# Kernel optimization log

Hardware: AMD Instinct MI355X
Metric: run time of the kernel (lower is better)

The kernel has to match this reference:

```python
import jax, jax.numpy as jnp
import numpy as np

B, N = 16, 8192

# batched gather: pts [N,C], ind [S,K] -> [S,K,C]
_bgather = jax.vmap(lambda pts, ind: pts[ind])


def _fps(xyz, npoint):
    """Farthest point sampling. xyz [B,N,3] -> idx [B,npoint] int32."""
    b, n, _ = xyz.shape
    def step(carry, _):
        mind, last = carry
        p = jax.vmap(lambda pts, i: pts[i])(xyz, last)  # [B,3]
        d = jnp.sum((xyz - p[:, None, :]) ** 2, axis=-1)  # [B,N]
        mind = jnp.minimum(mind, d)
        nxt = jnp.argmax(mind, axis=-1).astype(jnp.int32)
        return (mind, nxt), last
    init = (jnp.full((b, n), 1e10, xyz.dtype), jnp.zeros((b,), jnp.int32))
    _, idx = jax.lax.scan(step, init, None, length=npoint)
    return jnp.transpose(idx)  # [B,npoint]


def _ball_query(xyz, new_xyz, radius, nsample):
    """xyz [B,N,3], new_xyz [B,S,3] -> idx [B,S,nsample] int32.
    First nsample points within radius; slots past the count filled with first hit
    (matches pointnet2 CUDA ball_query semantics)."""
    n = xyz.shape[1]
    # squared distances without materializing [B,S,N,3]
    d2 = (jnp.sum(new_xyz ** 2, -1)[:, :, None]
          + jnp.sum(xyz ** 2, -1)[:, None, :]
          - 2.0 * jnp.einsum('bsc,bnc->bsn', new_xyz, xyz))  # [B,S,N]
    key = jnp.where(d2 < radius * radius, jnp.arange(n, dtype=jnp.int32), n)
    idx = jnp.sort(key, axis=-1)[..., :nsample]  # first in-radius indices
    first = idx[..., :1]
    idx = jnp.where(idx == n, first, idx)  # pad with first hit
    return jnp.clip(idx, 0, n - 1)


def _mlp(g, layers):
    # g [B,S,K,C]; shared 1x1-conv MLP with folded BN, ReLU
    for W, b in layers:
        g = jax.nn.relu(jnp.einsum('bskc,oc->bsko', g, W) + b)
    return g


def _sa(xyz, feat, npoint, radius, nsample, layers):
    fidx = _fps(xyz, npoint)
    new_xyz = _bgather(xyz, fidx)  # [B,S,3]
    idx = _ball_query(xyz, new_xyz, radius, nsample)  # [B,S,K]
    g = _bgather(xyz, idx) - new_xyz[:, :, None, :]  # centered grouped xyz
    if feat is not None:
        g = jnp.concatenate([g, _bgather(feat, idx)], axis=-1)
    g = _mlp(g, layers)
    return new_xyz, jnp.max(g, axis=2)  # [B,S,Cout]


def setup_inputs() -> dict:
    key = jax.random.key(0)
    ks = jax.random.split(key, 13)
    def w(k, o, i):
        return (jax.random.normal(k, (o, i), jnp.float32) * 0.1)
    inp = {
        'x': jax.random.uniform(ks[0], (B, N, 3), jnp.float32),
        'W1a': w(ks[1], 64, 3),    'b1a': jnp.zeros((64,), jnp.float32),
        'W1b': w(ks[2], 128, 64),  'b1b': jnp.zeros((128,), jnp.float32),
        'W2a': w(ks[3], 128, 131), 'b2a': jnp.zeros((128,), jnp.float32),
        'W2b': w(ks[4], 256, 128), 'b2b': jnp.zeros((256,), jnp.float32),
        'W3a': w(ks[5], 512, 259), 'b3a': jnp.zeros((512,), jnp.float32),
        'W3b': w(ks[6], 1024, 512),'b3b': jnp.zeros((1024,), jnp.float32),
    }
    return inp


def reference(x, W1a, b1a, W1b, b1b, W2a, b2a, W2b, b2b, W3a, b3a, W3b, b3b):
    xyz = x[..., 0:3]  # input_feat_dim=0 -> no extra features
    # sa1: npoint=512, r=0.2, k=64, mlp 3->64->128 (use_xyz)
    xyz1, feat1 = _sa(xyz, None, 512, 0.2, 64, [(W1a, b1a), (W1b, b1b)])
    # sa2: npoint=128, r=0.4, k=64, mlp 131->128->256
    xyz2, feat2 = _sa(xyz1, feat1, 128, 0.4, 64, [(W2a, b2a), (W2b, b2b)])
    # sa3: group-all, mlp 259->512->1024
    g = jnp.concatenate([xyz2, feat2], axis=-1)[:, None]  # [B,1,128,259]
    g = _mlp(g, [(W3a, b3a), (W3b, b3b)])
    return jnp.max(g, axis=2)[:, 0]  # [B,1024]
```

## Files before the change

kernel.cpp:

```cpp
#include <hip/hip_runtime.h>

#define B 16
#define N 8192
#define S1 512
#define S2 128
#define K 64

template<int CTRL>
__device__ __forceinline__ float dpp_max_f32(float v) {
  unsigned o = (unsigned)__builtin_amdgcn_update_dpp(
      (int)__float_as_uint(v), (int)__float_as_uint(v), CTRL, 0xF, 0xF, false);
  return fmaxf(v, __uint_as_float(o));
}

__device__ __forceinline__ float wave_max_bcast(float v) {
  v = dpp_max_f32<0x111>(v);
  v = dpp_max_f32<0x112>(v);
  v = dpp_max_f32<0x114>(v);
  v = dpp_max_f32<0x118>(v);
  v = dpp_max_f32<0x142>(v);
  v = dpp_max_f32<0x143>(v);
  return __uint_as_float((unsigned)__builtin_amdgcn_readlane(
      (int)__float_as_uint(v), 63));
}

template<int NT, int PT, int MAXP, int MAXN>
__device__ __forceinline__ void fps_body(
    const float* __restrict__ pts, float* __restrict__ out_xyz,
    float* __restrict__ out2, int out2_stride, int n, int npoint) {
  const int b = blockIdx.x;
  const int t = threadIdx.x;
  const int w = t >> 6;
  const float* base = pts + (size_t)b * n * 3;
  __shared__ unsigned long long cell[3][4];
  __shared__ float s_out[MAXP * 3];
  __shared__ float s_pts[MAXN * 3];
  if (t < 12) ((unsigned long long*)cell)[t] = 0ull;
  float px[PT], py[PT], pz[PT], mind[PT];
#pragma unroll
  for (int i = 0; i < PT; i++) {
    int p = t + i * NT;
    px[i] = base[p * 3 + 0];
    py[i] = base[p * 3 + 1];
    pz[i] = base[p * 3 + 2];
    mind[i] = 1e10f;
    s_pts[p * 3 + 0] = px[i];
    s_pts[p * 3 + 1] = py[i];
    s_pts[p * 3 + 2] = pz[i];
  }
  float cx = base[0], cy = base[1], cz = base[2];
  __syncthreads();
  for (int it = 0; it < npoint; it++) {
    if (t == 0) {
      s_out[it * 3 + 0] = cx; s_out[it * 3 + 1] = cy; s_out[it * 3 + 2] = cz;
    }
    float bv = -1.0f;
#pragma unroll
    for (int i = 0; i < PT; i++) {
      float dx = px[i] - cx, dy = py[i] - cy, dz = pz[i] - cz;
      float d = dx * dx;
      d = fmaf(dy, dy, d);
      d = fmaf(dz, dz, d);
      float md = fminf(mind[i], d);
      mind[i] = md;
      bv = fmaxf(bv, md);
    }
    float gm = wave_max_bcast(bv);
    if (bv == gm) {
      int bi = 0;
#pragma unroll
      for (int i = PT - 1; i >= 0; i--)
        if (mind[i] == bv) bi = i;
      unsigned long long kk = ((unsigned long long)__float_as_uint(bv) << 32) |
                              (~(unsigned)(t + bi * NT));
      atomicMax(&cell[it % 3][w & 3], kk);
    }
    if (t < 4) cell[(it + 1) % 3][t] = 0ull;
    __syncthreads();
    unsigned long long k0 = cell[it % 3][0];
    unsigned long long k1 = cell[it % 3][1];
    unsigned long long k2 = cell[it % 3][2];
    unsigned long long k3 = cell[it % 3][3];
    unsigned long long wk = k0 > k1 ? k0 : k1;
    unsigned long long wk2 = k2 > k3 ? k2 : k3;
    if (wk2 > wk) wk = wk2;
    int ui = __builtin_amdgcn_readfirstlane((int)(~(unsigned)wk));
    const float* q = s_pts + ui * 3;
    cx = q[0]; cy = q[1]; cz = q[2];
  }
  for (int e = t; e < npoint * 3; e += NT)
    out_xyz[(size_t)b * npoint * 3 + e] = s_out[e];
  if (out2) {
    for (int e = t; e < npoint; e += NT) {
      float* o2 = out2 + ((size_t)b * npoint + e) * out2_stride;
      o2[0] = s_out[e * 3 + 0];
      o2[1] = s_out[e * 3 + 1];
      o2[2] = s_out[e * 3 + 2];
    }
  }
}

__global__ __launch_bounds__(1024) __attribute__((amdgpu_waves_per_eu(4, 4)))
void fps1_kernel(const float* __restrict__ pts, float* __restrict__ out_xyz,
                 float* __restrict__ out2, int out2_stride, int n, int npoint) {
  fps_body<1024, 8, 512, 8192>(pts, out_xyz, out2, out2_stride, n, npoint);
}

template<int PT, int MAXP, int MAXN>
__global__ __launch_bounds__(64) __attribute__((amdgpu_waves_per_eu(1, 1)))
void fps_wave_kernel(const float* __restrict__ pts, float* __restrict__ out_xyz,
                     float* __restrict__ out2, int out2_stride, int n, int npoint) {
  const int b = blockIdx.x;
  const int t = threadIdx.x;
  const float* base = pts + (size_t)b * n * 3;
  __shared__ unsigned long long cell[2];
  __shared__ float s_out[MAXP * 3];
  __shared__ float s_pts[MAXN * 3];
  if (t < 2) cell[t] = 0ull;
  float px[PT], py[PT], pz[PT], mind[PT];
#pragma unroll
  for (int i = 0; i < PT; i++) {
    int p = t + i * 64;
    px[i] = base[p * 3 + 0];
    py[i] = base[p * 3 + 1];
    pz[i] = base[p * 3 + 2];
    mind[i] = 1e10f;
    s_pts[p * 3 + 0] = px[i];
    s_pts[p * 3 + 1] = py[i];
    s_pts[p * 3 + 2] = pz[i];
  }
  float cx = base[0], cy = base[1], cz = base[2];
  for (int it = 0; it < npoint; it++) {
    if (t == 0) {
      s_out[it * 3 + 0] = cx; s_out[it * 3 + 1] = cy; s_out[it * 3 + 2] = cz;
    }
    float bv = -1.0f;
#pragma unroll
    for (int i = 0; i < PT; i++) {
      float dx = px[i] - cx, dy = py[i] - cy, dz = pz[i] - cz;
      float d = dx * dx;
      d = fmaf(dy, dy, d);
      d = fmaf(dz, dz, d);
      float md = fminf(mind[i], d);
      mind[i] = md;
      bv = fmaxf(bv, md);
    }
    float gm = wave_max_bcast(bv);
    if (bv == gm) {
      int bi = 0;
#pragma unroll
      for (int i = PT - 1; i >= 0; i--)
        if (mind[i] == bv) bi = i;
      unsigned long long kk = ((unsigned long long)__float_as_uint(bv) << 32) |
                              (~(unsigned)(t + bi * 64));
      atomicMax(&cell[it & 1], kk);
    }
    __threadfence_block();
    unsigned long long wk = cell[it & 1];
    if (t == 0) cell[(it + 1) & 1] = 0ull;
    int ui = __builtin_amdgcn_readfirstlane((int)(~(unsigned)wk));
    const float* q = s_pts + ui * 3;
    cx = q[0]; cy = q[1]; cz = q[2];
  }
  for (int e = t; e < npoint * 3; e += 64)
    out_xyz[(size_t)b * npoint * 3 + e] = s_out[e];
  if (out2) {
    for (int e = t; e < npoint; e += 64) {
      float* o2 = out2 + ((size_t)b * npoint + e) * out2_stride;
      o2[0] = s_out[e * 3 + 0];
      o2[1] = s_out[e * 3 + 1];
      o2[2] = s_out[e * 3 + 2];
    }
  }
}

__global__ __launch_bounds__(256) void ballq_kernel(
    const float* __restrict__ pts, const float* __restrict__ ctr,
    int* __restrict__ idx, int n, int ns, int total, float r2) {
  int gid = blockIdx.x * blockDim.x + threadIdx.x;
  int wid = gid >> 6;
  int lane = threadIdx.x & 63;
  if (wid >= total) return;
  int b = wid / ns, s = wid - b * ns;
  const float* pb = pts + (size_t)b * n * 3;
  const float* c = ctr + ((size_t)b * ns + s) * 3;
  float cx = c[0], cy = c[1], cz = c[2];
  float sc = cx * cx + cy * cy + cz * cz;
  int* out = idx + ((size_t)b * ns + s) * K;
  int cnt = 0, first = n - 1;
  for (int base = 0; base < n && cnt < K; base += 64) {
    int p = base + lane;
    float x = pb[p * 3 + 0], y = pb[p * 3 + 1], z = pb[p * 3 + 2];
    float sp = x * x + y * y + z * z;
    float dot = cx * x + cy * y + cz * z;
    float d2 = sc + sp - 2.0f * dot;
    bool inr = d2 < r2;
    unsigned long long m = __ballot(inr);
    if (cnt == 0 && m != 0ull) first = base + __ffsll((long long)m) - 1;
    int pre = (int)__popcll(m & ((1ull << lane) - 1ull));
    if (inr && (cnt + pre) < K) out[cnt + pre] = p;
    cnt += (int)__popcll(m);
  }
  if (cnt > K) cnt = K;
  if (lane >= cnt) out[lane] = first;
}

__global__ __launch_bounds__(256) void sa1_kernel(
    const float* __restrict__ xyz, const int* __restrict__ idx,
    const float* __restrict__ ctr, const float* __restrict__ W1a,
    const float* __restrict__ b1a, const float* __restrict__ W1b,
    const float* __restrict__ b1b, float* __restrict__ feat) {
  __shared__ float s_l[K][3];
  __shared__ float s_h[K][64];
  __shared__ float s_red[128];
  int blk = blockIdx.x;
  int b = blk >> 9, s = blk & 511;
  int tid = threadIdx.x;
  const int* gi = idx + ((size_t)b * S1 + s) * K;
  const float* c = ctr + ((size_t)b * S1 + s) * 3;
  float cx = c[0], cy = c[1], cz = c[2];
  if (tid < K) {
    int p = gi[tid];
    const float* q = xyz + ((size_t)b * N + p) * 3;
    s_l[tid][0] = q[0] - cx;
    s_l[tid][1] = q[1] - cy;
    s_l[tid][2] = q[2] - cz;
  }
  __syncthreads();
  for (int e = tid; e < K * 64; e += 256) {
    int k = e >> 6, o = e & 63;
    float v = b1a[o] + W1a[o * 3 + 0] * s_l[k][0] + W1a[o * 3 + 1] * s_l[k][1] +
              W1a[o * 3 + 2] * s_l[k][2];
    s_h[k][o] = fmaxf(v, 0.f);
  }
  __syncthreads();
  int o = tid & 127, half = tid >> 7;
  float w[64];
  const float4* wp = (const float4*)(W1b + o * 64);
#pragma unroll
  for (int c4 = 0; c4 < 16; c4++) {
    float4 t4 = wp[c4];
    w[c4 * 4 + 0] = t4.x; w[c4 * 4 + 1] = t4.y;
    w[c4 * 4 + 2] = t4.z; w[c4 * 4 + 3] = t4.w;
  }
  float bias = b1b[o];
  float m = -1e30f;
  int k0 = half * 32;
  for (int k = k0; k < k0 + 32; k++) {
    float acc = bias;
    const float4* hp = (const float4*)(&s_h[k][0]);
#pragma unroll
    for (int c4 = 0; c4 < 16; c4++) {
      float4 h = hp[c4];
      acc = fmaf(h.x, w[c4 * 4 + 0], acc);
      acc = fmaf(h.y, w[c4 * 4 + 1], acc);
      acc = fmaf(h.z, w[c4 * 4 + 2], acc);
      acc = fmaf(h.w, w[c4 * 4 + 3], acc);
    }
    m = fmaxf(m, acc);
  }
  if (half == 1) s_red[o] = m;
  __syncthreads();
  if (half == 0) {
    m = fmaxf(m, s_red[o]);
    feat[((size_t)b * S1 + s) * 128 + o] = fmaxf(m, 0.f);
  }
}

__global__ __launch_bounds__(256) void sa2_kernel(
    const float* __restrict__ xyz1, const float* __restrict__ feat1,
    const int* __restrict__ idx, const float* __restrict__ ctr,
    const float* __restrict__ W2a, const float* __restrict__ b2a,
    const float* __restrict__ W2b, const float* __restrict__ b2b,
    float* __restrict__ in3) {
  __shared__ int s_pi[K];
  __shared__ float s_g[K][132];
  __shared__ float s_h[K][128];
  __shared__ float s_red[256];
  int blk = blockIdx.x;
  int b = blk >> 7, s = blk & 127;
  int tid = threadIdx.x;
  const int* gi = idx + ((size_t)b * S2 + s) * K;
  const float* c = ctr + ((size_t)b * S2 + s) * 3;
  float cx = c[0], cy = c[1], cz = c[2];
  if (tid < K) {
    int p = gi[tid];
    s_pi[tid] = p;
    const float* q = xyz1 + ((size_t)b * S1 + p) * 3;
    s_g[tid][0] = q[0] - cx;
    s_g[tid][1] = q[1] - cy;
    s_g[tid][2] = q[2] - cz;
  }
  __syncthreads();
  for (int e = tid; e < K * 128; e += 256) {
    int k = e >> 7, f = e & 127;
    s_g[k][3 + f] = feat1[((size_t)b * S1 + s_pi[k]) * 128 + f];
  }
  __syncthreads();
  {
    int o = tid & 127, half = tid >> 7, k0 = half * 32;
    const float* wr = W2a + o * 131;
    float acc[32];
    float bias = b2a[o];
#pragma unroll
    for (int j = 0; j < 32; j++) acc[j] = bias;
    for (int c4 = 0; c4 < 32; c4++) {
      float w0 = wr[c4 * 4 + 0], w1 = wr[c4 * 4 + 1];
      float w2 = wr[c4 * 4 + 2], w3 = wr[c4 * 4 + 3];
#pragma unroll
      for (int j = 0; j < 32; j++) {
        float4 g = *(const float4*)(&s_g[k0 + j][c4 * 4]);
        acc[j] = fmaf(g.x, w0, acc[j]);
        acc[j] = fmaf(g.y, w1, acc[j]);
        acc[j] = fmaf(g.z, w2, acc[j]);
        acc[j] = fmaf(g.w, w3, acc[j]);
      }
    }
    float w0 = wr[128], w1 = wr[129], w2 = wr[130];
#pragma unroll
    for (int j = 0; j < 32; j++) {
      acc[j] = fmaf(s_g[k0 + j][128], w0, acc[j]);
      acc[j] = fmaf(s_g[k0 + j][129], w1, acc[j]);
      acc[j] = fmaf(s_g[k0 + j][130], w2, acc[j]);
      s_h[k0 + j][o] = fmaxf(acc[j], 0.f);
    }
  }
  __syncthreads();
  {
    int oa = tid & 127, half = tid >> 7, k0 = half * 32;
    const float4* wpa = (const float4*)(W2b + oa * 128);
    const float4* wpb = (const float4*)(W2b + (oa + 128) * 128);
    float acca[32], accb[32];
    float ba = b2b[oa], bb = b2b[oa + 128];
#pragma unroll
    for (int j = 0; j < 32; j++) { acca[j] = ba; accb[j] = bb; }
    for (int c4 = 0; c4 < 32; c4++) {
      float4 wa = wpa[c4];
      float4 wb = wpb[c4];
#pragma unroll
      for (int j = 0; j < 32; j++) {
        float4 h = *(const float4*)(&s_h[k0 + j][c4 * 4]);
        acca[j] = fmaf(h.x, wa.x, acca[j]);
        acca[j] = fmaf(h.y, wa.y, acca[j]);
        acca[j] = fmaf(h.z, wa.z, acca[j]);
        acca[j] = fmaf(h.w, wa.w, acca[j]);
        accb[j] = fmaf(h.x, wb.x, accb[j]);
        accb[j] = fmaf(h.y, wb.y, accb[j]);
        accb[j] = fmaf(h.z, wb.z, accb[j]);
        accb[j] = fmaf(h.w, wb.w, accb[j]);
      }
    }
    float ma = -1e30f, mb = -1e30f;
#pragma unroll
    for (int j = 0; j < 32; j++) { ma = fmaxf(ma, acca[j]); mb = fmaxf(mb, accb[j]); }
    if (half == 1) { s_red[oa] = ma; s_red[oa + 128] = mb; }
    __syncthreads();
    if (half == 0) {
      ma = fmaxf(ma, s_red[oa]);
      mb = fmaxf(mb, s_red[oa + 128]);
      float* o3 = &in3[((size_t)b * S2 + s) * 259 + 3];
      o3[oa] = fmaxf(ma, 0.f);
      o3[oa + 128] = fmaxf(mb, 0.f);
    }
  }
}

__global__ __launch_bounds__(256) void mlp3a_kernel(
    const float* __restrict__ in3, const float* __restrict__ W3a,
    const float* __restrict__ b3a, float* __restrict__ h3) {
  __shared__ float s_wt[64][65];
  __shared__ float s_a[64][64];
  int blk = blockIdx.x;
  int b = blk >> 4, r = blk & 15;
  int ot = r >> 1, sh = r & 1;
  int tid = threadIdx.x;
  int o = tid & 63, sq = tid >> 6;
  float acc[16];
  float bias = b3a[ot * 64 + o];
#pragma unroll
  for (int j = 0; j < 16; j++) acc[j] = bias;
  for (int ch = 0; ch < 5; ch++) {
    int cb = ch * 64;
    int len = (ch == 4) ? 3 : 64;
    for (int e = tid; e < 4096; e += 256) {
      int oo = e >> 6, cc = e & 63;
      if (cc < len) s_wt[cc][oo] = W3a[(size_t)(ot * 64 + oo) * 259 + cb + cc];
    }
    for (int e = tid; e < 4096; e += 256) {
      int ss = e >> 6, cc = e & 63;
      if (cc < len) s_a[ss][cc] = in3[((size_t)b * S2 + sh * 64 + ss) * 259 + cb + cc];
    }
    __syncthreads();
    for (int cc = 0; cc < len; cc++) {
      float wv = s_wt[cc][o];
#pragma unroll
      for (int j = 0; j < 16; j++)
        acc[j] = fmaf(wv, s_a[sq * 16 + j][cc], acc[j]);
    }
    __syncthreads();
  }
#pragma unroll
  for (int j = 0; j < 16; j++) {
    int s = sh * 64 + sq * 16 + j;
    h3[((size_t)b * S2 + s) * 512 + ot * 64 + o] = fmaxf(acc[j], 0.f);
  }
}

__global__ __launch_bounds__(256) void mlp3b_kernel(
    const float* __restrict__ h3, const float* __restrict__ W3b,
    const float* __restrict__ b3b, float* __restrict__ out) {
  __shared__ float s_wt[64][65];
  __shared__ float s_h[128][64];
  __shared__ float s_red[4][64];
  int blk = blockIdx.x;
  int b = blk >> 4, ot = blk & 15;
  int tid = threadIdx.x;
  int o = tid & 63, sq = tid >> 6;
  float acc[32];
  float bias = b3b[ot * 64 + o];
#pragma unroll
  for (int j = 0; j < 32; j++) acc[j] = bias;
  for (int ch = 0; ch < 8; ch++) {
    int cb = ch * 64;
    for (int e = tid; e < 4096; e += 256) {
      int oo = e >> 6, cc = e & 63;
      s_wt[cc][oo] = W3b[(size_t)(ot * 64 + oo) * 512 + cb + cc];
    }
    for (int e = tid; e < 8192; e += 256) {
      int ss = e >> 6, cc = e & 63;
      s_h[ss][cc] = h3[((size_t)b * S2 + ss) * 512 + cb + cc];
    }
    __syncthreads();
    for (int c4 = 0; c4 < 16; c4++) {
      float w0 = s_wt[c4 * 4 + 0][o];
      float w1 = s_wt[c4 * 4 + 1][o];
      float w2 = s_wt[c4 * 4 + 2][o];
      float w3 = s_wt[c4 * 4 + 3][o];
#pragma unroll
      for (int j = 0; j < 32; j++) {
        float4 h = *(const float4*)(&s_h[sq * 32 + j][c4 * 4]);
        acc[j] = fmaf(h.x, w0, acc[j]);
        acc[j] = fmaf(h.y, w1, acc[j]);
        acc[j] = fmaf(h.z, w2, acc[j]);
        acc[j] = fmaf(h.w, w3, acc[j]);
      }
    }
    __syncthreads();
  }
  float m = -1e30f;
#pragma unroll
  for (int j = 0; j < 32; j++) m = fmaxf(m, acc[j]);
  s_red[sq][o] = m;
  __syncthreads();
  if (sq == 0) {
    m = fmaxf(fmaxf(s_red[0][o], s_red[1][o]), fmaxf(s_red[2][o], s_red[3][o]));
    out[(size_t)b * 1024 + ot * 64 + o] = fmaxf(m, 0.f);
  }
}

extern "C" void kernel_launch(void* const* d_in, const int* in_sizes, int n_in,
                              void* d_out, int out_size, void* d_ws, size_t ws_size,
                              hipStream_t stream) {
  const float* x = (const float*)d_in[0];
  const float* W1a = (const float*)d_in[1];
  const float* b1a = (const float*)d_in[2];
  const float* W1b = (const float*)d_in[3];
  const float* b1b = (const float*)d_in[4];
  const float* W2a = (const float*)d_in[5];
  const float* b2a = (const float*)d_in[6];
  const float* W2b = (const float*)d_in[7];
  const float* b2b = (const float*)d_in[8];
  const float* W3a = (const float*)d_in[9];
  const float* b3a = (const float*)d_in[10];
  const float* W3b = (const float*)d_in[11];
  const float* b3b = (const float*)d_in[12];
  float* out = (float*)d_out;

  float* nx1 = (float*)d_ws;
  int* idx1 = (int*)(nx1 + 16 * 512 * 3);
  float* feat1 = (float*)(idx1 + 16 * 512 * 64);
  float* nx2 = feat1 + 16 * 512 * 128;
  int* idx2 = (int*)(nx2 + 16 * 128 * 3);
  float* in3 = (float*)(idx2 + 16 * 128 * 64);
  float* h3 = in3 + 16 * 128 * 259;

  fps1_kernel<<<B, 1024, 0, stream>>>(x, nx1, nullptr, 0, N, S1);
  ballq_kernel<<<(B * S1) / 4, 256, 0, stream>>>(x, nx1, idx1, N, S1, B * S1, 0.04f);
  sa1_kernel<<<B * S1, 256, 0, stream>>>(x, idx1, nx1, W1a, b1a, W1b, b1b, feat1);
  fps_wave_kernel<8, 128, 512><<<B, 64, 0, stream>>>(nx1, nx2, in3, 259, S1, S2);
  ballq_kernel<<<(B * S2) / 4, 256, 0, stream>>>(nx1, nx2, idx2, S1, S2, B * S2, 0.16f);
  sa2_kernel<<<B * S2, 256, 0, stream>>>(nx1, feat1, idx2, nx2, W2a, b2a, W2b, b2b, in3);
  mlp3a_kernel<<<256, 256, 0, stream>>>(in3, W3a, b3a, h3);
  mlp3b_kernel<<<256, 256, 0, stream>>>(h3, W3b, b3b, out);
}
```

Baseline: 1.372 ms.

## Fuse ball query into SA1 and SA2 kernels with 4-wave split scan

Removes the separate ball-query kernels and runs the neighbour search inside the SA1/SA2 blocks. Each of the four waves scans a quarter of the point set into a shared hit list, and the lists are merged in order. This drops two launches and the global index round trip. The cost is that every wave scans up to its own 64 hits, so total scan work can rise when the early points are dense, and the search now sits in front of the MLP in the same block.

```diff
diff --git a/kernel.cpp b/kernel.cpp
--- a/kernel.cpp
+++ b/kernel.cpp
@@ -174,21 +174,16 @@
   }
 }
 
-__global__ __launch_bounds__(256) void ballq_kernel(
-    const float* __restrict__ pts, const float* __restrict__ ctr,
-    int* __restrict__ idx, int n, int ns, int total, float r2) {
-  int gid = blockIdx.x * blockDim.x + threadIdx.x;
-  int wid = gid >> 6;
-  int lane = threadIdx.x & 63;
-  if (wid >= total) return;
-  int b = wid / ns, s = wid - b * ns;
-  const float* pb = pts + (size_t)b * n * 3;
-  const float* c = ctr + ((size_t)b * ns + s) * 3;
-  float cx = c[0], cy = c[1], cz = c[2];
-  float sc = cx * cx + cy * cy + cz * cz;
-  int* out = idx + ((size_t)b * ns + s) * K;
-  int cnt = 0, first = n - 1;
-  for (int base = 0; base < n && cnt < K; base += 64) {
+template<int NPTS>
+__device__ __forceinline__ int ballq_fused(
+    const float* __restrict__ pb, float cx, float cy, float cz, float r2,
+    int tid, int* s_hits , int* s_cnt , int* s_first ) {
+  const int w = tid >> 6, lane = tid & 63;
+  const float sc = cx * cx + cy * cy + cz * cz;
+  constexpr int QUARTER = NPTS / 4;
+  int cnt = 0, first = 0x7fffffff;
+  const int qbase = w * QUARTER;
+  for (int base = qbase; base < qbase + QUARTER && cnt < K; base += 64) {
     int p = base + lane;
     float x = pb[p * 3 + 0], y = pb[p * 3 + 1], z = pb[p * 3 + 2];
     float sp = x * x + y * y + z * z;
@@ -196,32 +191,52 @@
     float d2 = sc + sp - 2.0f * dot;
     bool inr = d2 < r2;
     unsigned long long m = __ballot(inr);
-    if (cnt == 0 && m != 0ull) first = base + __ffsll((long long)m) - 1;
+    if (first == 0x7fffffff && m != 0ull) first = base + __ffsll((long long)m) - 1;
     int pre = (int)__popcll(m & ((1ull << lane) - 1ull));
-    if (inr && (cnt + pre) < K) out[cnt + pre] = p;
+    if (inr && (cnt + pre) < K) s_hits[w * K + cnt + pre] = p;
     cnt += (int)__popcll(m);
   }
-  if (cnt > K) cnt = K;
-  if (lane >= cnt) out[lane] = first;
+  if (lane == 0) { s_cnt[w] = cnt; s_first[w] = first; }
+  __syncthreads();
+  int cc0 = s_cnt[0] < K ? s_cnt[0] : K;
+  int cc1 = s_cnt[1] < K ? s_cnt[1] : K;
+  int cc2 = s_cnt[2] < K ? s_cnt[2] : K;
+  int cc3 = s_cnt[3] < K ? s_cnt[3] : K;
+  int k = tid;
+  int idxk;
+  if (k < cc0) idxk = s_hits[0 * K + k];
+  else if (k < cc0 + cc1) idxk = s_hits[1 * K + k - cc0];
+  else if (k < cc0 + cc1 + cc2) idxk = s_hits[2 * K + k - cc0 - cc1];
+  else if (k < cc0 + cc1 + cc2 + cc3) idxk = s_hits[3 * K + k - cc0 - cc1 - cc2];
+  else {
+    int f01 = s_first[0] < s_first[1] ? s_first[0] : s_first[1];
+    int f23 = s_first[2] < s_first[3] ? s_first[2] : s_first[3];
+    int f = f01 < f23 ? f01 : f23;
+    idxk = (f == 0x7fffffff) ? (NPTS - 1) : f;
+  }
+  return idxk;
 }
 
 __global__ __launch_bounds__(256) void sa1_kernel(
-    const float* __restrict__ xyz, const int* __restrict__ idx,
-    const float* __restrict__ ctr, const float* __restrict__ W1a,
-    const float* __restrict__ b1a, const float* __restrict__ W1b,
-    const float* __restrict__ b1b, float* __restrict__ feat) {
+    const float* __restrict__ xyz, const float* __restrict__ ctr,
+    const float* __restrict__ W1a, const float* __restrict__ b1a,
+    const float* __restrict__ W1b, const float* __restrict__ b1b,
+    float* __restrict__ feat) {
+  __shared__ int s_hits[4 * K];
+  __shared__ int s_cnt[4];
+  __shared__ int s_first[4];
   __shared__ float s_l[K][3];
   __shared__ float s_h[K][64];
   __shared__ float s_red[128];
   int blk = blockIdx.x;
   int b = blk >> 9, s = blk & 511;
   int tid = threadIdx.x;
-  const int* gi = idx + ((size_t)b * S1 + s) * K;
   const float* c = ctr + ((size_t)b * S1 + s) * 3;
   float cx = c[0], cy = c[1], cz = c[2];
+  const float* pb = xyz + (size_t)b * N * 3;
+  int idxk = ballq_fused<N>(pb, cx, cy, cz, 0.04f, tid, s_hits, s_cnt, s_first);
   if (tid < K) {
-    int p = gi[tid];
-    const float* q = xyz + ((size_t)b * N + p) * 3;
+    const float* q = pb + (size_t)idxk * 3;
     s_l[tid][0] = q[0] - cx;
     s_l[tid][1] = q[1] - cy;
     s_l[tid][2] = q[2] - cz;
@@ -269,10 +284,13 @@
 
 __global__ __launch_bounds__(256) void sa2_kernel(
     const float* __restrict__ xyz1, const float* __restrict__ feat1,
-    const int* __restrict__ idx, const float* __restrict__ ctr,
+    const float* __restrict__ ctr,
     const float* __restrict__ W2a, const float* __restrict__ b2a,
     const float* __restrict__ W2b, const float* __restrict__ b2b,
     float* __restrict__ in3) {
+  __shared__ int s_hits[4 * K];
+  __shared__ int s_cnt[4];
+  __shared__ int s_first[4];
   __shared__ int s_pi[K];
   __shared__ float s_g[K][132];
   __shared__ float s_h[K][128];
@@ -280,13 +298,13 @@
   int blk = blockIdx.x;
   int b = blk >> 7, s = blk & 127;
   int tid = threadIdx.x;
-  const int* gi = idx + ((size_t)b * S2 + s) * K;
   const float* c = ctr + ((size_t)b * S2 + s) * 3;
   float cx = c[0], cy = c[1], cz = c[2];
+  const float* pb = xyz1 + (size_t)b * S1 * 3;
+  int idxk = ballq_fused<S1>(pb, cx, cy, cz, 0.16f, tid, s_hits, s_cnt, s_first);
   if (tid < K) {
-    int p = gi[tid];
-    s_pi[tid] = p;
-    const float* q = xyz1 + ((size_t)b * S1 + p) * 3;
+    s_pi[tid] = idxk;
+    const float* q = pb + (size_t)idxk * 3;
     s_g[tid][0] = q[0] - cx;
     s_g[tid][1] = q[1] - cy;
     s_g[tid][2] = q[2] - cz;
@@ -477,19 +495,15 @@
   float* out = (float*)d_out;
 
   float* nx1 = (float*)d_ws;
-  int* idx1 = (int*)(nx1 + 16 * 512 * 3);
-  float* feat1 = (float*)(idx1 + 16 * 512 * 64);
+  float* feat1 = nx1 + 16 * 512 * 3;
   float* nx2 = feat1 + 16 * 512 * 128;
-  int* idx2 = (int*)(nx2 + 16 * 128 * 3);
-  float* in3 = (float*)(idx2 + 16 * 128 * 64);
+  float* in3 = nx2 + 16 * 128 * 3;
   float* h3 = in3 + 16 * 128 * 259;
 
   fps1_kernel<<<B, 1024, 0, stream>>>(x, nx1, nullptr, 0, N, S1);
-  ballq_kernel<<<(B * S1) / 4, 256, 0, stream>>>(x, nx1, idx1, N, S1, B * S1, 0.04f);
-  sa1_kernel<<<B * S1, 256, 0, stream>>>(x, idx1, nx1, W1a, b1a, W1b, b1b, feat1);
+  sa1_kernel<<<B * S1, 256, 0, stream>>>(x, nx1, W1a, b1a, W1b, b1b, feat1);
   fps_wave_kernel<8, 128, 512><<<B, 64, 0, stream>>>(nx1, nx2, in3, 259, S1, S2);
-  ballq_kernel<<<(B * S2) / 4, 256, 0, stream>>>(nx1, nx2, idx2, S1, S2, B * S2, 0.16f);
-  sa2_kernel<<<B * S2, 256, 0, stream>>>(nx1, feat1, idx2, nx2, W2a, b2a, W2b, b2b, in3);
+  sa2_kernel<<<B * S2, 256, 0, stream>>>(nx1, feat1, nx2, W2a, b2a, W2b, b2b, in3);
   mlp3a_kernel<<<256, 256, 0, stream>>>(in3, W3a, b3a, h3);
   mlp3b_kernel<<<256, 256, 0, stream>>>(h3, W3b, b3b, out);
 }
```

Result: slower. 1.481 ms (+7.9%).
